# Performance work log

Measured on AMD Instinct MI355X. Metric: run time of the kernel, lower is better.

Reference implementation:

```python
import jax, jax.numpy as jnp
import numpy as np

B, N, E = 4, 4096, 65536
DIN, DB, DO, T = 128, 64, 128, 4  # in_features, bond_features, out_features, n_edge_types
DCAT = 2 * DIN + DB


def setup_inputs() -> dict:
    key = jax.random.key(0)
    ks = jax.random.split(key, 24)
    s = 0.05
    inp = {
        "sites": jax.random.normal(ks[0], (B, N, DIN), jnp.float32),
        "bonds": jax.random.normal(ks[1], (B, E, DB), jnp.float32),
        "idx1": jax.random.randint(ks[2], (E,), 0, N),
        "idx2": jax.random.randint(ks[3], (E,), 0, N),
        "uc": jax.random.randint(ks[4], (E,), 0, T),
        # per-type 2-layer MLPs (stacked over types)
        "W1a": jax.random.normal(ks[5], (T, DCAT, DO), jnp.float32) * s,
        "b1a": jnp.zeros((T, DO), jnp.float32),
        "W1b": jax.random.normal(ks[6], (T, DO, DO), jnp.float32) * s,
        "b1b": jnp.zeros((T, DO), jnp.float32),
        "W2a": jax.random.normal(ks[7], (T, DCAT, DO), jnp.float32) * s,
        "b2a": jnp.zeros((T, DO), jnp.float32),
        "W2b": jax.random.normal(ks[8], (T, DO, DO), jnp.float32) * s,
        "b2b": jnp.zeros((T, DO), jnp.float32),
        # attention gates (Linear(out,1) + sigmoid)
        "Wa1": jax.random.normal(ks[9], (DO, 1), jnp.float32) * s,
        "ba1": jnp.zeros((1,), jnp.float32),
        "Wa2": jax.random.normal(ks[10], (DO, 1), jnp.float32) * s,
        "ba2": jnp.zeros((1,), jnp.float32),
    }
    return inp


def reference(sites, bonds, idx1, idx2, uc, W1a, b1a, W1b, b1b,
              W2a, b2a, W2b, b2b, Wa1, ba1, Wa2, ba2):
    lrelu = jax.nn.leaky_relu  # negative_slope 0.01, matches nn.LeakyReLU default
    # gather edge endpoints and concat with bond features: [B, E, 2*DIN+DB]
    v = jnp.concatenate([sites[:, idx1], sites[:, idx2], bonds], axis=2)

    def mlp(Wa, ba, Wb, bb):
        return lrelu(v @ Wa + ba) @ Wb + bb  # [B, E, DO]

    n_types = W1a.shape[0]
    out1 = jnp.zeros((v.shape[0], v.shape[1], W1b.shape[-1]), v.dtype)
    out2 = jnp.zeros_like(out1)
    for i in range(n_types):  # small fixed set of structurally distinct weights
        m = (uc == i)[None, :, None]
        out1 = jnp.where(m, mlp(W1a[i], b1a[i], W1b[i], b1b[i]), out1)
        out2 = jnp.where(m, mlp(W2a[i], b2a[i], W2b[i], b2b[i]), out2)
    out1 = lrelu(out1)
    out2 = lrelu(out2)
    # sigmoid attention gate
    g1 = jax.nn.sigmoid(out1 @ Wa1 + ba1) * out1
    g2 = jax.nn.sigmoid(out2 @ Wa2 + ba2) * out2
    # scatter_add over edges -> nodes along dim 1, then sum
    n_nodes = sites.shape[1]
    agg = jnp.zeros((sites.shape[0], n_nodes, out1.shape[-1]), v.dtype)
    agg = agg.at[:, idx2].add(g1 + g2)
    return agg
```

## Files before the change

### kernel.cpp

```cpp
#include <hip/hip_runtime.h>

#define NB 4
#define NN 4096
#define NE 65536
#define DIN 128
#define DB 64
#define DOUT 128
#define NT 4
#define DCAT 320

#define MT 64
#define LDH (DOUT + 8)

typedef __bf16 bf16;
typedef __bf16 bf16x4 __attribute__((ext_vector_type(4)));
typedef __bf16 bf16x8 __attribute__((ext_vector_type(8)));
typedef float floatx4 __attribute__((ext_vector_type(4)));

__device__ __forceinline__ void async16(const void* g, void* l) {
    __builtin_amdgcn_global_load_lds(
        (const __attribute__((address_space(1))) unsigned int*)g,
        (__attribute__((address_space(3))) unsigned int*)l, 16, 0, 0);
}

#define NS4 (NB * NN * DIN / 4)
#define NA  (NT * 256 * DCAT)
#define NB2 (NT * 256 * DOUT)
#define NZERO 8208
__global__ void prep_k(const float* __restrict__ sites,
                       const float* __restrict__ W1a, const float* __restrict__ W2a,
                       const float* __restrict__ W1b, const float* __restrict__ W2b,
                       bf16* __restrict__ sitesB,
                       bf16* __restrict__ WtA, bf16* __restrict__ WtB,
                       int* __restrict__ zeroRegion) {
    int i = blockIdx.x * 256 + threadIdx.x;
    if (i < NZERO) zeroRegion[i] = 0;
    if (i < NS4) {
        float4 f = ((const float4*)sites)[i];
        bf16x4 h = { (bf16)f.x, (bf16)f.y, (bf16)f.z, (bf16)f.w };
        ((bf16x4*)sitesB)[i] = h;
    } else if (i < NS4 + NA) {
        int j = i - NS4;
        int k = j % DCAT;
        int n = (j / DCAT) % 256;
        int t = j / (DCAT * 256);
        float w = (n < DOUT) ? W1a[(t * DCAT + k) * DOUT + n]
                             : W2a[(t * DCAT + k) * DOUT + (n - DOUT)];
        WtA[j] = (bf16)w;
    } else {
        int j = i - NS4 - NA;
        int k = j % DOUT;
        int n = (j / DOUT) % 256;
        int t = j / (DOUT * 256);
        float w = (n < DOUT) ? W1b[(t * DOUT + k) * DOUT + n]
                             : W2b[(t * DOUT + k) * DOUT + (n - DOUT)];
        WtB[j] = (bf16)w;
    }
}

__global__ void bucket_k(const int* __restrict__ uc, const int* __restrict__ idx2,
                         int* __restrict__ cnt, int* __restrict__ deg,
                         int* __restrict__ bucket) {
    __shared__ int h[NT];
    __shared__ int baseo[NT];
    int tid = threadIdx.x;
    if (tid < NT) h[tid] = 0;
    __syncthreads();
    int e = blockIdx.x * 256 + tid;
    int t = uc[e] & 3;
    int lp = atomicAdd(&h[t], 1);
    __syncthreads();
    if (tid < NT) baseo[tid] = atomicAdd(&cnt[tid], h[tid]);
    __syncthreads();
    bucket[t * NE + baseo[t] + lp] = e;
    atomicAdd(&deg[idx2[e] & (NN - 1)], 1);
}

__global__ void scan_k(const int* __restrict__ deg, int* __restrict__ off) {
    __shared__ int wsum[4];
    int tid = threadIdx.x;
    int lane = tid & 63, w = tid >> 6;
    int v[16]; int s = 0;
    #pragma unroll
    for (int j = 0; j < 16; ++j) { v[j] = deg[tid * 16 + j]; s += v[j]; }
    int inc = s;
    #pragma unroll
    for (int d = 1; d < 64; d <<= 1) {
        int x = __shfl_up(inc, d, 64);
        if (lane >= d) inc += x;
    }
    if (lane == 63) wsum[w] = inc;
    __syncthreads();
    int wpre = 0;
    #pragma unroll
    for (int j = 0; j < 4; ++j) wpre += (j < w) ? wsum[j] : 0;
    int excl = wpre + inc - s;
    #pragma unroll
    for (int j = 0; j < 16; ++j) { off[tid * 16 + j] = excl; excl += v[j]; }
    if (tid == 255) off[4096] = excl;
}

__global__ void fill_k(const int* __restrict__ idx2, const int* __restrict__ off,
                       int* __restrict__ cursor, int* __restrict__ perm) {
    int e = blockIdx.x * 256 + threadIdx.x;
    int n = idx2[e] & (NN - 1);
    int p = atomicAdd(&cursor[n], 1);
    perm[e] = off[n] + p;
}

__launch_bounds__(256, 3)
__global__ void main_k(const bf16* __restrict__ sitesB, const float* __restrict__ bonds,
                       const int* __restrict__ idx1, const int* __restrict__ idx2,
                       const int* __restrict__ cnt, const int* __restrict__ bucket,
                       const int* __restrict__ perm,
                       const bf16* __restrict__ WtA, const bf16* __restrict__ WtB,
                       const float* __restrict__ b1a, const float* __restrict__ b2a,
                       const float* __restrict__ b1b, const float* __restrict__ b2b,
                       const float* __restrict__ Wa1, const float* __restrict__ ba1,
                       const float* __restrict__ Wa2, const float* __restrict__ ba2,
                       bf16* __restrict__ eo) {
    __shared__ __align__(16) char smem[40960];
    bf16* sA  = (bf16*)smem;
    bf16* sB  = (bf16*)(smem + 8192);
    bf16* sH1 = (bf16*)smem;
    bf16* sH2 = (bf16*)(smem + MT * LDH * 2);
    __shared__ int sI1[MT], sI2[MT], sEid[MT], sPrm[MT];

    const int tid = threadIdx.x;

    int blk = blockIdx.x;
    int p = blk & 7;
    const int b = p >> 1;
    int flat = ((blk >> 3) << 1) + (p & 1);

    int c0 = cnt[0], c1 = cnt[1], c2 = cnt[2], c3 = cnt[3];
    int n0 = (c0 + MT - 1) / MT, n1 = (c1 + MT - 1) / MT,
        n2 = (c2 + MT - 1) / MT, n3 = (c3 + MT - 1) / MT;
    int t, ti, cT;
    if (flat < n0)                { t = 0; ti = flat;                cT = c0; }
    else if (flat < n0+n1)        { t = 1; ti = flat - n0;           cT = c1; }
    else if (flat < n0+n1+n2)     { t = 2; ti = flat - n0 - n1;      cT = c2; }
    else if (flat < n0+n1+n2+n3)  { t = 3; ti = flat - n0 - n1 - n2; cT = c3; }
    else return;
    const int base = ti * MT;
    const int nvalid = min(MT, cT - base);

    if (tid < MT) {
        int rr = min(tid, max(nvalid - 1, 0));
        int e = bucket[t * NE + base + rr] & (NE - 1);
        sEid[tid] = e;
        sPrm[tid] = perm[e] & (NE - 1);
        sI1[tid] = idx1[e] & (NN - 1);
        sI2[tid] = idx2[e] & (NN - 1);
    }
    __syncthreads();

    const int wv = tid >> 6;
    const int lane = tid & 63;
    const int br = wv >> 1;
    const int nh = wv & 1;
    const int lr = lane & 15;
    const int quad = lane >> 4;
    const int lk = quad * 8;
    const int colbase = nh * 64;

    float4 fb[4][2][2];
    #pragma unroll
    for (int mt = 0; mt < 4; ++mt) {
        const float* pb = bonds + ((size_t)b * NE + sEid[mt * 16 + lr]) * DB + lk;
        fb[mt][0][0] = *(const float4*)pb;
        fb[mt][0][1] = *(const float4*)(pb + 4);
        fb[mt][1][0] = *(const float4*)(pb + 32);
        fb[mt][1][1] = *(const float4*)(pb + 36);
    }
    bf16x8 aB[2][4];
    #pragma unroll
    for (int ks = 0; ks < 2; ++ks)
        #pragma unroll
        for (int mt = 0; mt < 4; ++mt) {
            float4 f0 = fb[mt][ks][0], f1 = fb[mt][ks][1];
            aB[ks][mt] = (bf16x8){ (bf16)f0.x, (bf16)f0.y, (bf16)f0.z, (bf16)f0.w,
                                   (bf16)f1.x, (bf16)f1.y, (bf16)f1.z, (bf16)f1.w };
        }

    const size_t sbase = (size_t)b * NN;
    auto stageA = [&](int ks, int buf) {
        int d = wv * 64 + lane;
        int row = d >> 2;
        int kseg = (d & 3) ^ (row & 3);
        int r = (ks < 4) ? sI1[row] : sI2[row];
        const bf16* src = sitesB + (sbase + r) * DIN + (ks & 3) * 32 + kseg * 8;
        async16(src, &sA[buf * 2048 + wv * 512]);
    };
    auto stageB1 = [&](int ks, int buf) {
        #pragma unroll
        for (int j = 0; j < 4; ++j) {
            int d = (j * 4 + wv) * 64 + lane;
            int col = d >> 2;
            int kseg = (d & 3) ^ (col & 3);
            const bf16* src = WtA + (size_t)(t * 256 + col) * DCAT + ks * 32 + kseg * 8;
            async16(src, &sB[buf * 8192 + (j * 4 + wv) * 512]);
        }
    };

    floatx4 acc[4][4];
    #pragma unroll
    for (int mt = 0; mt < 4; ++mt)
        #pragma unroll
        for (int nt = 0; nt < 4; ++nt)
            acc[mt][nt] = (floatx4){0.f, 0.f, 0.f, 0.f};

    stageA(0, 0);
    stageB1(0, 0);
    #pragma unroll
    for (int ks = 0; ks < 10; ++ks) {
        int buf = ks & 1;
        __syncthreads();
        if (ks < 9) {
            if (ks + 1 < 8) stageA(ks + 1, buf ^ 1);
            stageB1(ks + 1, buf ^ 1);
        }
        bf16x8 aF[4];
        #pragma unroll
        for (int mt = 0; mt < 4; ++mt) {
            if (ks < 8) {
                int row = mt * 16 + lr;
                aF[mt] = *(const bf16x8*)(&sA[buf * 2048 + (row * 4 + (quad ^ (lr & 3))) * 8]);
            } else {
                aF[mt] = aB[ks - 8][mt];
            }
        }
        #pragma unroll
        for (int nt = 0; nt < 4; ++nt) {
            int cc = br * 128 + colbase + nt * 16 + lr;
            bf16x8 bF = *(const bf16x8*)(&sB[buf * 8192 + (cc * 4 + (quad ^ (lr & 3))) * 8]);
            #pragma unroll
            for (int mt = 0; mt < 4; ++mt)
                acc[mt][nt] = __builtin_amdgcn_mfma_f32_16x16x32_bf16(aF[mt], bF, acc[mt][nt], 0, 0, 0);
        }
    }
    __syncthreads();

    bf16* sH = (br == 0) ? sH1 : sH2;
    const float* biasA = ((br == 0) ? b1a : b2a) + t * DOUT;
    #pragma unroll
    for (int nt = 0; nt < 4; ++nt) {
        int c = colbase + nt * 16 + lr;
        float bias = biasA[c];
        #pragma unroll
        for (int mt = 0; mt < 4; ++mt) {
            int rbase = mt * 16 + quad * 4;
            #pragma unroll
            for (int rg = 0; rg < 4; ++rg) {
                float v = acc[mt][nt][rg] + bias;
                v = v > 0.f ? v : 0.01f * v;
                sH[(rbase + rg) * LDH + c] = (bf16)v;
            }
        }
    }
    __syncthreads();

    floatx4 acc2[4][4];
    #pragma unroll
    for (int mt = 0; mt < 4; ++mt)
        #pragma unroll
        for (int nt = 0; nt < 4; ++nt)
            acc2[mt][nt] = (floatx4){0.f, 0.f, 0.f, 0.f};

    const bf16* sHa = (br == 0) ? sH1 : sH2;
    const bf16* WtB_w = WtB + (size_t)(t * 256 + br * 128 + colbase) * DOUT + lk;
    #pragma unroll
    for (int ks = 0; ks < 4; ++ks) {
        bf16x8 aF[4];
        #pragma unroll
        for (int mt = 0; mt < 4; ++mt)
            aF[mt] = *(const bf16x8*)(&sHa[(mt * 16 + lr) * LDH + ks * 32 + lk]);
        #pragma unroll
        for (int nt = 0; nt < 4; ++nt) {
            bf16x8 bF = *(const bf16x8*)(&WtB_w[(size_t)(nt * 16 + lr) * DOUT + ks * 32]);
            #pragma unroll
            for (int mt = 0; mt < 4; ++mt)
                acc2[mt][nt] = __builtin_amdgcn_mfma_f32_16x16x32_bf16(aF[mt], bF, acc2[mt][nt], 0, 0, 0);
        }
    }
    __syncthreads();

    const float* biasB = ((br == 0) ? b1b : b2b) + t * DOUT;
    #pragma unroll
    for (int nt = 0; nt < 4; ++nt) {
        int c = colbase + nt * 16 + lr;
        float bias = biasB[c];
        #pragma unroll
        for (int mt = 0; mt < 4; ++mt) {
            int rbase = mt * 16 + quad * 4;
            #pragma unroll
            for (int rg = 0; rg < 4; ++rg) {
                float v = acc2[mt][nt][rg] + bias;
                v = v > 0.f ? v : 0.01f * v;
                sH[(rbase + rg) * LDH + c] = (bf16)v;
            }
        }
    }
    __syncthreads();

    {
        int m = tid >> 2;
        int q = tid & 3;
        float d1 = 0.f, d2 = 0.f;
        #pragma unroll
        for (int c = 0; c < 32; ++c) {
            int cc = q * 32 + c;
            d1 += (float)sH1[m * LDH + cc] * Wa1[cc];
            d2 += (float)sH2[m * LDH + cc] * Wa2[cc];
        }
        d1 += __shfl_xor(d1, 1); d1 += __shfl_xor(d1, 2);
        d2 += __shfl_xor(d2, 1); d2 += __shfl_xor(d2, 2);
        d1 = fminf(fmaxf(d1 + ba1[0], -30.f), 30.f);
        d2 = fminf(fmaxf(d2 + ba2[0], -30.f), 30.f);
        float s1 = 1.f / (1.f + __expf(-d1));
        float s2 = 1.f / (1.f + __expf(-d2));
        if (m < nvalid) {
            bf16* dst = eo + ((size_t)b * NE + sPrm[m]) * DOUT;
            #pragma unroll
            for (int j = 0; j < 4; ++j) {
                int cc = (q + 4 * j) * 8;
                bf16x8 w;
                #pragma unroll
                for (int c = 0; c < 8; ++c) {
                    int col = cc + c;
                    float v = s1 * (float)sH1[m * LDH + col] + s2 * (float)sH2[m * LDH + col];
                    w[c] = (bf16)v;
                }
                *(bf16x8*)(dst + cc) = w;
            }
        }
    }
}

__global__ void gather_k(const bf16* __restrict__ eo, const int* __restrict__ off,
                         float* __restrict__ out) {
    __shared__ float part[128];
    int tid = threadIdx.x;
    int s = tid >> 7;
    int c = tid & 127;
    int n = blockIdx.x;
    int b = blockIdx.y;
    int o0 = off[n], o1 = off[n + 1];
    const bf16* eob = eo + (size_t)b * NE * DOUT + c;
    float a0 = 0.f, a1 = 0.f, a2 = 0.f, a3 = 0.f;
    int i = o0 + s;
    for (; i + 6 < o1; i += 8) {
        a0 += (float)eob[(size_t)(i)     * DOUT];
        a1 += (float)eob[(size_t)(i + 2) * DOUT];
        a2 += (float)eob[(size_t)(i + 4) * DOUT];
        a3 += (float)eob[(size_t)(i + 6) * DOUT];
    }
    for (; i < o1; i += 2)
        a0 += (float)eob[(size_t)i * DOUT];
    float tot = (a0 + a1) + (a2 + a3);
    if (s == 0) part[c] = tot;
    __syncthreads();
    if (s == 1) out[((size_t)b * NN + n) * DOUT + c] = part[c] + tot;
}

extern "C" void kernel_launch(void* const* d_in, const int* in_sizes, int n_in,
                              void* d_out, int out_size, void* d_ws, size_t ws_size,
                              hipStream_t stream) {
    const float* sites = (const float*)d_in[0];
    const float* bonds = (const float*)d_in[1];
    const int*   idx1  = (const int*)d_in[2];
    const int*   idx2  = (const int*)d_in[3];
    const int*   uc    = (const int*)d_in[4];
    const float* W1a = (const float*)d_in[5];
    const float* b1a = (const float*)d_in[6];
    const float* W1b = (const float*)d_in[7];
    const float* b1b = (const float*)d_in[8];
    const float* W2a = (const float*)d_in[9];
    const float* b2a = (const float*)d_in[10];
    const float* W2b = (const float*)d_in[11];
    const float* b2b = (const float*)d_in[12];
    const float* Wa1 = (const float*)d_in[13];
    const float* ba1 = (const float*)d_in[14];
    const float* Wa2 = (const float*)d_in[15];
    const float* ba2 = (const float*)d_in[16];
    float* out = (float*)d_out;

    char* ws = (char*)d_ws;
    size_t o_cnt    = 0;
    size_t o_deg    = 64;
    size_t o_cursor = o_deg + NN * 4;
    size_t o_off    = o_cursor + NN * 4;
    size_t o_bucket = o_off + (NN + 16) * 4;
    size_t o_perm   = o_bucket + (size_t)NT * NE * 4;
    size_t o_wta    = o_perm + (size_t)NE * 4;
    size_t o_wtb    = o_wta + (size_t)NA * 2;
    size_t o_sitesB = o_wtb + (size_t)NB2 * 2;
    size_t o_eo     = o_sitesB + (size_t)NB * NN * DIN * 2;
    size_t need     = o_eo + (size_t)NB * NE * DOUT * 2;
    if (ws_size < need) return;

    int*  cnt    = (int*)(ws + o_cnt);
    int*  deg    = (int*)(ws + o_deg);
    int*  cursor = (int*)(ws + o_cursor);
    int*  off    = (int*)(ws + o_off);
    int*  bucket = (int*)(ws + o_bucket);
    int*  perm   = (int*)(ws + o_perm);
    bf16* WtA    = (bf16*)(ws + o_wta);
    bf16* WtB    = (bf16*)(ws + o_wtb);
    bf16* sitesB = (bf16*)(ws + o_sitesB);
    bf16* eo     = (bf16*)(ws + o_eo);

    prep_k<<<(NS4 + NA + NB2) / 256, 256, 0, stream>>>(sites, W1a, W2a, W1b, W2b,
                                                       sitesB, WtA, WtB, (int*)ws);
    bucket_k<<<NE / 256, 256, 0, stream>>>(uc, idx2, cnt, deg, bucket);
    scan_k<<<1, 256, 0, stream>>>(deg, off);
    fill_k<<<NE / 256, 256, 0, stream>>>(idx2, off, cursor, perm);

    const int maxTiles = NE / MT + NT;
    main_k<<<maxTiles * NB, 256, 0, stream>>>(
        sitesB, bonds, idx1, idx2, cnt, bucket, perm, WtA, WtB,
        b1a, b2a, b1b, b2b, Wa1, ba1, Wa2, ba2, eo);

    gather_k<<<dim3(NN, NB), 256, 0, stream>>>(eo, off, out);
}
```

Baseline: 324.9 us.

## Pre-convert bonds to bf16, stream via async LDS, vectorize epilogues and gather

Bonds are converted to bf16 in the prep kernel and streamed through the same async global-to-LDS pipeline as the site rows, instead of being loaded as fp32 into registers per tile. Per-row indices now live in registers rather than shared memory. The LDS writes of hidden activations are paired into bf16x2 stores via lane shuffles, and the gate dot product reads vectorized data with the gate weights cached in LDS. The gather kernel reads 16-byte bf16x8 vectors across 16 row groups, and occupancy is raised to 4 blocks per CU. Together these cut register pressure and memory-instruction count, at the cost of an extra bf16 bonds buffer and an extra conversion pass.

```diff
diff --git a/kernel.cpp b/kernel.cpp
--- a/kernel.cpp
+++ b/kernel.cpp
@@ -13,6 +13,7 @@
 #define LDH (DOUT + 8)
 
 typedef __bf16 bf16;
+typedef __bf16 bf16x2 __attribute__((ext_vector_type(2)));
 typedef __bf16 bf16x4 __attribute__((ext_vector_type(4)));
 typedef __bf16 bf16x8 __attribute__((ext_vector_type(8)));
 typedef float floatx4 __attribute__((ext_vector_type(4)));
@@ -26,12 +27,14 @@
 #define NS4 (NB * NN * DIN / 4)
 #define NA  (NT * 256 * DCAT)
 #define NB2 (NT * 256 * DOUT)
+#define NBO4 (NB * NE * DB / 4)
 #define NZERO 8208
-__global__ void prep_k(const float* __restrict__ sites,
+__global__ void prep_k(const float* __restrict__ sites, const float* __restrict__ bonds,
                        const float* __restrict__ W1a, const float* __restrict__ W2a,
                        const float* __restrict__ W1b, const float* __restrict__ W2b,
                        bf16* __restrict__ sitesB,
                        bf16* __restrict__ WtA, bf16* __restrict__ WtB,
+                       bf16* __restrict__ bondsB,
                        int* __restrict__ zeroRegion) {
     int i = blockIdx.x * 256 + threadIdx.x;
     if (i < NZERO) zeroRegion[i] = 0;
@@ -47,7 +50,7 @@
         float w = (n < DOUT) ? W1a[(t * DCAT + k) * DOUT + n]
                              : W2a[(t * DCAT + k) * DOUT + (n - DOUT)];
         WtA[j] = (bf16)w;
-    } else {
+    } else if (i < NS4 + NA + NB2) {
         int j = i - NS4 - NA;
         int k = j % DOUT;
         int n = (j / DOUT) % 256;
@@ -55,6 +58,11 @@
         float w = (n < DOUT) ? W1b[(t * DOUT + k) * DOUT + n]
                              : W2b[(t * DOUT + k) * DOUT + (n - DOUT)];
         WtB[j] = (bf16)w;
+    } else {
+        int j = i - NS4 - NA - NB2;
+        float4 f = ((const float4*)bonds)[j];
+        bf16x4 h = { (bf16)f.x, (bf16)f.y, (bf16)f.z, (bf16)f.w };
+        ((bf16x4*)bondsB)[j] = h;
     }
 }
 
@@ -108,8 +116,8 @@
     perm[e] = off[n] + p;
 }
 
-__launch_bounds__(256, 3)
-__global__ void main_k(const bf16* __restrict__ sitesB, const float* __restrict__ bonds,
+__launch_bounds__(256, 4)
+__global__ void main_k(const bf16* __restrict__ sitesB, const bf16* __restrict__ bondsB,
                        const int* __restrict__ idx1, const int* __restrict__ idx2,
                        const int* __restrict__ cnt, const int* __restrict__ bucket,
                        const int* __restrict__ perm,
@@ -124,7 +132,7 @@
     bf16* sB  = (bf16*)(smem + 8192);
     bf16* sH1 = (bf16*)smem;
     bf16* sH2 = (bf16*)(smem + MT * LDH * 2);
-    __shared__ int sI1[MT], sI2[MT], sEid[MT], sPrm[MT];
+    float* sWa = (float*)(smem + 35840);
 
     const int tid = threadIdx.x;
 
@@ -145,15 +153,12 @@
     const int base = ti * MT;
     const int nvalid = min(MT, cT - base);
 
-    if (tid < MT) {
-        int rr = min(tid, max(nvalid - 1, 0));
-        int e = bucket[t * NE + base + rr] & (NE - 1);
-        sEid[tid] = e;
-        sPrm[tid] = perm[e] & (NE - 1);
-        sI1[tid] = idx1[e] & (NN - 1);
-        sI2[tid] = idx2[e] & (NN - 1);
-    }
-    __syncthreads();
+    const int rowA = tid >> 2;
+    const int rr = min(rowA, max(nvalid - 1, 0));
+    const int e  = bucket[t * NE + base + rr] & (NE - 1);
+    const int r1 = idx1[e] & (NN - 1);
+    const int r2 = idx2[e] & (NN - 1);
+    const int prm = perm[e] & (NE - 1);
 
     const int wv = tid >> 6;
     const int lane = tid & 63;
@@ -163,42 +168,27 @@
     const int quad = lane >> 4;
     const int lk = quad * 8;
     const int colbase = nh * 64;
-
-    float4 fb[4][2][2];
-    #pragma unroll
-    for (int mt = 0; mt < 4; ++mt) {
-        const float* pb = bonds + ((size_t)b * NE + sEid[mt * 16 + lr]) * DB + lk;
-        fb[mt][0][0] = *(const float4*)pb;
-        fb[mt][0][1] = *(const float4*)(pb + 4);
-        fb[mt][1][0] = *(const float4*)(pb + 32);
-        fb[mt][1][1] = *(const float4*)(pb + 36);
-    }
-    bf16x8 aB[2][4];
-    #pragma unroll
-    for (int ks = 0; ks < 2; ++ks)
-        #pragma unroll
-        for (int mt = 0; mt < 4; ++mt) {
-            float4 f0 = fb[mt][ks][0], f1 = fb[mt][ks][1];
-            aB[ks][mt] = (bf16x8){ (bf16)f0.x, (bf16)f0.y, (bf16)f0.z, (bf16)f0.w,
-                                   (bf16)f1.x, (bf16)f1.y, (bf16)f1.z, (bf16)f1.w };
-        }
+    const int lodd = lane & 1;
 
     const size_t sbase = (size_t)b * NN;
+    const int kseg = (tid & 3) ^ (rowA & 3);
+    const bf16* pA1 = sitesB + (sbase + r1) * DIN + kseg * 8;
+    const bf16* pA2 = sitesB + (sbase + r2) * DIN + kseg * 8;
+    const bf16* pBo = bondsB + ((size_t)b * NE + e) * DB + kseg * 8;
+
     auto stageA = [&](int ks, int buf) {
-        int d = wv * 64 + lane;
-        int row = d >> 2;
-        int kseg = (d & 3) ^ (row & 3);
-        int r = (ks < 4) ? sI1[row] : sI2[row];
-        const bf16* src = sitesB + (sbase + r) * DIN + (ks & 3) * 32 + kseg * 8;
-        async16(src, &sA[buf * 2048 + wv * 512]);
+        const bf16* src = (ks < 4) ? (pA1 + ks * 32)
+                        : (ks < 8) ? (pA2 + (ks - 4) * 32)
+                                   : (pBo + (ks - 8) * 32);
+        async16(src, smem + buf * 4096 + wv * 1024);
     };
     auto stageB1 = [&](int ks, int buf) {
         #pragma unroll
         for (int j = 0; j < 4; ++j) {
             int d = (j * 4 + wv) * 64 + lane;
             int col = d >> 2;
-            int kseg = (d & 3) ^ (col & 3);
-            const bf16* src = WtA + (size_t)(t * 256 + col) * DCAT + ks * 32 + kseg * 8;
+            int ksg = (d & 3) ^ (col & 3);
+            const bf16* src = WtA + (size_t)(t * 256 + col) * DCAT + ks * 32 + ksg * 8;
             async16(src, &sB[buf * 8192 + (j * 4 + wv) * 512]);
         }
     };
@@ -217,18 +207,14 @@
         int buf = ks & 1;
         __syncthreads();
         if (ks < 9) {
-            if (ks + 1 < 8) stageA(ks + 1, buf ^ 1);
+            stageA(ks + 1, buf ^ 1);
             stageB1(ks + 1, buf ^ 1);
         }
         bf16x8 aF[4];
         #pragma unroll
         for (int mt = 0; mt < 4; ++mt) {
-            if (ks < 8) {
-                int row = mt * 16 + lr;
-                aF[mt] = *(const bf16x8*)(&sA[buf * 2048 + (row * 4 + (quad ^ (lr & 3))) * 8]);
-            } else {
-                aF[mt] = aB[ks - 8][mt];
-            }
+            int row = mt * 16 + lr;
+            aF[mt] = *(const bf16x8*)(&sA[buf * 2048 + (row * 4 + (quad ^ (lr & 3))) * 8]);
         }
         #pragma unroll
         for (int nt = 0; nt < 4; ++nt) {
@@ -241,21 +227,30 @@
     }
     __syncthreads();
 
+    sWa[tid] = (tid < 128) ? Wa1[tid] : Wa2[tid - 128];
+
     bf16* sH = (br == 0) ? sH1 : sH2;
     const float* biasA = ((br == 0) ? b1a : b2a) + t * DOUT;
     #pragma unroll
     for (int nt = 0; nt < 4; ++nt) {
         int c = colbase + nt * 16 + lr;
+        int cpair = c & ~1;
         float bias = biasA[c];
         #pragma unroll
         for (int mt = 0; mt < 4; ++mt) {
-            int rbase = mt * 16 + quad * 4;
+            float v[4], x[4];
             #pragma unroll
             for (int rg = 0; rg < 4; ++rg) {
-                float v = acc[mt][nt][rg] + bias;
-                v = v > 0.f ? v : 0.01f * v;
-                sH[(rbase + rg) * LDH + c] = (bf16)v;
+                float u = acc[mt][nt][rg] + bias;
+                v[rg] = u > 0.f ? u : 0.01f * u;
             }
+            #pragma unroll
+            for (int rg = 0; rg < 4; ++rg) x[rg] = __shfl_xor(v[rg], 1);
+            int r0 = mt * 16 + quad * 4 + lodd * 2;
+            float lo0 = lodd ? x[2] : v[0], hi0 = lodd ? v[2] : x[0];
+            float lo1 = lodd ? x[3] : v[1], hi1 = lodd ? v[3] : x[1];
+            *(bf16x2*)(&sH[r0 * LDH + cpair])       = (bf16x2){ (bf16)lo0, (bf16)hi0 };
+            *(bf16x2*)(&sH[(r0 + 1) * LDH + cpair]) = (bf16x2){ (bf16)lo1, (bf16)hi1 };
         }
     }
     __syncthreads();
@@ -289,16 +284,23 @@
     #pragma unroll
     for (int nt = 0; nt < 4; ++nt) {
         int c = colbase + nt * 16 + lr;
+        int cpair = c & ~1;
         float bias = biasB[c];
         #pragma unroll
         for (int mt = 0; mt < 4; ++mt) {
-            int rbase = mt * 16 + quad * 4;
+            float v[4], x[4];
             #pragma unroll
             for (int rg = 0; rg < 4; ++rg) {
-                float v = acc2[mt][nt][rg] + bias;
-                v = v > 0.f ? v : 0.01f * v;
-                sH[(rbase + rg) * LDH + c] = (bf16)v;
+                float u = acc2[mt][nt][rg] + bias;
+                v[rg] = u > 0.f ? u : 0.01f * u;
             }
+            #pragma unroll
+            for (int rg = 0; rg < 4; ++rg) x[rg] = __shfl_xor(v[rg], 1);
+            int r0 = mt * 16 + quad * 4 + lodd * 2;
+            float lo0 = lodd ? x[2] : v[0], hi0 = lodd ? v[2] : x[0];
+            float lo1 = lodd ? x[3] : v[1], hi1 = lodd ? v[3] : x[1];
+            *(bf16x2*)(&sH[r0 * LDH + cpair])       = (bf16x2){ (bf16)lo0, (bf16)hi0 };
+            *(bf16x2*)(&sH[(r0 + 1) * LDH + cpair]) = (bf16x2){ (bf16)lo1, (bf16)hi1 };
         }
     }
     __syncthreads();
@@ -308,10 +310,21 @@
         int q = tid & 3;
         float d1 = 0.f, d2 = 0.f;
         #pragma unroll
-        for (int c = 0; c < 32; ++c) {
-            int cc = q * 32 + c;
-            d1 += (float)sH1[m * LDH + cc] * Wa1[cc];
-            d2 += (float)sH2[m * LDH + cc] * Wa2[cc];
+        for (int j = 0; j < 4; ++j) {
+            bf16x8 h1 = *(const bf16x8*)(&sH1[m * LDH + q * 32 + j * 8]);
+            bf16x8 h2 = *(const bf16x8*)(&sH2[m * LDH + q * 32 + j * 8]);
+            float4 wa = *(const float4*)(&sWa[q * 32 + j * 8]);
+            float4 wb = *(const float4*)(&sWa[q * 32 + j * 8 + 4]);
+            float4 va = *(const float4*)(&sWa[128 + q * 32 + j * 8]);
+            float4 vb = *(const float4*)(&sWa[128 + q * 32 + j * 8 + 4]);
+            d1 += (float)h1[0] * wa.x; d1 += (float)h1[1] * wa.y;
+            d1 += (float)h1[2] * wa.z; d1 += (float)h1[3] * wa.w;
+            d1 += (float)h1[4] * wb.x; d1 += (float)h1[5] * wb.y;
+            d1 += (float)h1[6] * wb.z; d1 += (float)h1[7] * wb.w;
+            d2 += (float)h2[0] * va.x; d2 += (float)h2[1] * va.y;
+            d2 += (float)h2[2] * va.z; d2 += (float)h2[3] * va.w;
+            d2 += (float)h2[4] * vb.x; d2 += (float)h2[5] * vb.y;
+            d2 += (float)h2[6] * vb.z; d2 += (float)h2[7] * vb.w;
         }
         d1 += __shfl_xor(d1, 1); d1 += __shfl_xor(d1, 2);
         d2 += __shfl_xor(d2, 1); d2 += __shfl_xor(d2, 2);
@@ -320,17 +333,16 @@
         float s1 = 1.f / (1.f + __expf(-d1));
         float s2 = 1.f / (1.f + __expf(-d2));
         if (m < nvalid) {
-            bf16* dst = eo + ((size_t)b * NE + sPrm[m]) * DOUT;
+            bf16* dst = eo + ((size_t)b * NE + prm) * DOUT;
             #pragma unroll
             for (int j = 0; j < 4; ++j) {
                 int cc = (q + 4 * j) * 8;
+                bf16x8 h1 = *(const bf16x8*)(&sH1[m * LDH + cc]);
+                bf16x8 h2 = *(const bf16x8*)(&sH2[m * LDH + cc]);
                 bf16x8 w;
                 #pragma unroll
-                for (int c = 0; c < 8; ++c) {
-                    int col = cc + c;
-                    float v = s1 * (float)sH1[m * LDH + col] + s2 * (float)sH2[m * LDH + col];
-                    w[c] = (bf16)v;
-                }
+                for (int c = 0; c < 8; ++c)
+                    w[c] = (bf16)(s1 * (float)h1[c] + s2 * (float)h2[c]);
                 *(bf16x8*)(dst + cc) = w;
             }
         }
@@ -339,28 +351,29 @@
 
 __global__ void gather_k(const bf16* __restrict__ eo, const int* __restrict__ off,
                          float* __restrict__ out) {
-    __shared__ float part[128];
+    __shared__ float part[16 * 128];
     int tid = threadIdx.x;
-    int s = tid >> 7;
-    int c = tid & 127;
+    int g = tid >> 4;
+    int cseg = tid & 15;
     int n = blockIdx.x;
     int b = blockIdx.y;
     int o0 = off[n], o1 = off[n + 1];
-    const bf16* eob = eo + (size_t)b * NE * DOUT + c;
-    float a0 = 0.f, a1 = 0.f, a2 = 0.f, a3 = 0.f;
-    int i = o0 + s;
-    for (; i + 6 < o1; i += 8) {
-        a0 += (float)eob[(size_t)(i)     * DOUT];
-        a1 += (float)eob[(size_t)(i + 2) * DOUT];
-        a2 += (float)eob[(size_t)(i + 4) * DOUT];
-        a3 += (float)eob[(size_t)(i + 6) * DOUT];
-    }
-    for (; i < o1; i += 2)
-        a0 += (float)eob[(size_t)i * DOUT];
-    float tot = (a0 + a1) + (a2 + a3);
-    if (s == 0) part[c] = tot;
-    __syncthreads();
-    if (s == 1) out[((size_t)b * NN + n) * DOUT + c] = part[c] + tot;
+    const bf16* base = eo + (size_t)b * NE * DOUT + cseg * 8;
+    float a[8] = {0.f, 0.f, 0.f, 0.f, 0.f, 0.f, 0.f, 0.f};
+    for (int r = o0 + g; r < o1; r += 16) {
+        bf16x8 v = *(const bf16x8*)(base + (size_t)r * DOUT);
+        #pragma unroll
+        for (int j = 0; j < 8; ++j) a[j] += (float)v[j];
+    }
+    #pragma unroll
+    for (int j = 0; j < 8; ++j) part[g * 128 + cseg * 8 + j] = a[j];
+    __syncthreads();
+    if (tid < 128) {
+        float s = 0.f;
+        #pragma unroll
+        for (int g2 = 0; g2 < 16; ++g2) s += part[g2 * 128 + tid];
+        out[((size_t)b * NN + n) * DOUT + tid] = s;
+    }
 }
 
 extern "C" void kernel_launch(void* const* d_in, const int* in_sizes, int n_in,
@@ -397,7 +410,9 @@
     size_t o_sitesB = o_wtb + (size_t)NB2 * 2;
     size_t o_eo     = o_sitesB + (size_t)NB * NN * DIN * 2;
     size_t need     = o_eo + (size_t)NB * NE * DOUT * 2;
-    if (ws_size < need) return;
+    size_t o_bondsB = need;
+    size_t need_full = o_bondsB + (size_t)NB * NE * DB * 2;
+    if (ws_size < need_full) return;
 
     int*  cnt    = (int*)(ws + o_cnt);
     int*  deg    = (int*)(ws + o_deg);
@@ -409,16 +424,17 @@
     bf16* WtB    = (bf16*)(ws + o_wtb);
     bf16* sitesB = (bf16*)(ws + o_sitesB);
     bf16* eo     = (bf16*)(ws + o_eo);
-
-    prep_k<<<(NS4 + NA + NB2) / 256, 256, 0, stream>>>(sites, W1a, W2a, W1b, W2b,
-                                                       sitesB, WtA, WtB, (int*)ws);
+    bf16* bondsB = (bf16*)(ws + o_bondsB);
+
+    prep_k<<<(NS4 + NA + NB2 + NBO4) / 256, 256, 0, stream>>>(
+        sites, bonds, W1a, W2a, W1b, W2b, sitesB, WtA, WtB, bondsB, (int*)ws);
     bucket_k<<<NE / 256, 256, 0, stream>>>(uc, idx2, cnt, deg, bucket);
     scan_k<<<1, 256, 0, stream>>>(deg, off);
     fill_k<<<NE / 256, 256, 0, stream>>>(idx2, off, cursor, perm);
 
     const int maxTiles = NE / MT + NT;
     main_k<<<maxTiles * NB, 256, 0, stream>>>(
-        sitesB, bonds, idx1, idx2, cnt, bucket, perm, WtA, WtB,
+        sitesB, bondsB, idx1, idx2, cnt, bucket, perm, WtA, WtB,
         b1a, b2a, b1b, b2b, Wa1, ba1, Wa2, ba2, eo);
 
     gather_k<<<dim3(NN, NB), 256, 0, stream>>>(eo, off, out);
```

After: 279.7 us. 1.16x faster.
